# Optimization experiments

Measured on AMD Instinct MI355X. Metric: run time of the kernel, lower is better.

Reference implementation:

```python
import jax, jax.numpy as jnp
import numpy as np
from jax.experimental.ode import odeint

B, N, D, META, H, OUT = 512, 64, 4, 4, 512, 1
RTOL, ATOL = 1e-3, 1e-5


def setup_inputs() -> dict:
    key = jax.random.key(0)
    ks = jax.random.split(key, 20)
    # x channel 0 = strictly increasing event times per sample (TIME), rest randn
    dt = jax.random.uniform(ks[0], (B, N), dtype=jnp.float32) * 0.1 + 0.01
    times = jnp.cumsum(dt, axis=1)
    feats = jax.random.normal(ks[1], (B, N, D - 1), dtype=jnp.float32)
    x = jnp.concatenate([times[..., None], feats], axis=-1)
    meta = jax.random.normal(ks[2], (B, META), dtype=jnp.float32)
    eps = jax.random.normal(ks[3], (B, H), dtype=jnp.float32)

    DIN = D + META
    s_in = 1.0 / np.sqrt(DIN)
    s_h = 1.0 / np.sqrt(H)
    p = {
        # GRU (torch layout: gates [r, z, n] stacked)
        'gru_Wih': jax.random.normal(ks[4], (3 * H, DIN), jnp.float32) * s_in,
        'gru_Whh': jax.random.normal(ks[5], (3 * H, H), jnp.float32) * s_h,
        'gru_bih': jax.random.normal(ks[6], (3 * H,), jnp.float32) * s_h,
        'gru_bhh': jax.random.normal(ks[7], (3 * H,), jnp.float32) * s_h,
        # encoder head: Linear(H,H) -> ReLU -> Linear(H,2H)
        'enc_W1': jax.random.normal(ks[8], (H, H), jnp.float32) * s_h,
        'enc_b1': jax.random.normal(ks[9], (H,), jnp.float32) * s_h,
        'enc_W2': jax.random.normal(ks[10], (2 * H, H), jnp.float32) * s_h,
        'enc_b2': jax.random.normal(ks[11], (2 * H,), jnp.float32) * s_h,
        # ODE drift net: Linear(H,H) -> SELU -> Linear(H,H); scaled mild for stable dynamics
        'ode_W1': jax.random.normal(ks[12], (H, H), jnp.float32) * (0.5 * s_h),
        'ode_b1': jax.random.normal(ks[13], (H,), jnp.float32) * 0.05,
        'ode_W2': jax.random.normal(ks[14], (H, H), jnp.float32) * (0.5 * s_h),
        'ode_b2': jax.random.normal(ks[15], (H,), jnp.float32) * 0.05,
        # output head: Linear(H+META, OUT)
        'fc_W': jax.random.normal(ks[16], (OUT, H + META), jnp.float32) / np.sqrt(H + META),
        'fc_b': jax.random.normal(ks[17], (OUT,), jnp.float32) / np.sqrt(H + META),
    }
    return {'x': x, 'meta': meta, 'eps': eps, **p}


def _gru_last(xm, Wih, Whh, bih, bhh):
    # xm: (B, N, DIN) -> final hidden state (B, H), torch nn.GRU equations
    def step(h, x_t):
        gi = x_t @ Wih.T + bih            # (B, 3H)
        gh = h @ Whh.T + bhh              # (B, 3H)
        i_r, i_z, i_n = jnp.split(gi, 3, axis=-1)
        h_r, h_z, h_n = jnp.split(gh, 3, axis=-1)
        r = jax.nn.sigmoid(i_r + h_r)
        z = jax.nn.sigmoid(i_z + h_z)
        n = jnp.tanh(i_n + r * h_n)
        return (1.0 - z) * n + z * h, None
    h0 = jnp.zeros((xm.shape[0], Whh.shape[1]), xm.dtype)
    h, _ = jax.lax.scan(step, h0, jnp.swapaxes(xm, 0, 1))
    return h


def reference(x, meta, eps, gru_Wih, gru_Whh, gru_bih, gru_bhh,
              enc_W1, enc_b1, enc_W2, enc_b2,
              ode_W1, ode_b1, ode_W2, ode_b2, fc_W, fc_b):
    times = x[:, :, 0]                                        # (B, N)
    metat = jnp.broadcast_to(meta[:, None, :], (x.shape[0], x.shape[1], meta.shape[1]))
    xm = jnp.concatenate([x, metat], axis=-1)                 # (B, N, D+META)
    h = _gru_last(xm, gru_Wih, gru_Whh, gru_bih, gru_bhh)     # (B, H)
    out = jax.nn.relu(h @ enc_W1.T + enc_b1) @ enc_W2.T + enc_b2
    mean, std = out[:, :H], out[:, H:]
    z0 = eps * std + mean                                     # reparameterized sample

    def drift(z, t, W1, b1, W2, b2):
        return jax.nn.selu(z @ W1.T + b1) @ W2.T + b2

    def solve_one(z0_b, t_b):
        return odeint(drift, z0_b, t_b, ode_W1, ode_b1, ode_W2, ode_b2,
                      rtol=RTOL, atol=ATOL)                   # (N, H)

    solves = jax.vmap(solve_one)(z0, times)                   # (B, N, H)
    latent = jnp.concatenate([solves[:, -1, :], meta], axis=-1)
    return latent @ fc_W.T + fc_b                             # (B, OUT)
```

## Files before the change

### kernel.cpp

```cpp
#include <hip/hip_runtime.h>
#include <math.h>

constexpr int Bsz  = 512;
constexpr int Nseq = 64;
constexpr int DX   = 4;
constexpr int MET  = 4;
constexpr int Hd   = 512;
constexpr int H3d  = 1536;

constexpr int PJ = 520;

constexpr float RTOL_C = 1e-3f;
constexpr float ATOL_C = 1e-5f;

constexpr float SB10 = (float)(1.0/5.0);
constexpr float SB20 = (float)(3.0/40.0),  SB21 = (float)(9.0/40.0);
constexpr float SB30 = (float)(44.0/45.0), SB31 = (float)(-56.0/15.0), SB32 = (float)(32.0/9.0);
constexpr float SB40 = (float)(19372.0/6561.0), SB41 = (float)(-25360.0/2187.0),
                SB42 = (float)(64448.0/6561.0), SB43 = (float)(-212.0/729.0);
constexpr float SB50 = (float)(9017.0/3168.0),  SB51 = (float)(-355.0/33.0),
                SB52 = (float)(46732.0/5247.0), SB53 = (float)(49.0/176.0),
                SB54 = (float)(-5103.0/18656.0);
constexpr float CS0 = (float)(35.0/384.0), CS2 = (float)(500.0/1113.0),
                CS3 = (float)(125.0/192.0), CS4 = (float)(-2187.0/6784.0),
                CS5 = (float)(11.0/84.0);
constexpr float CE0 = (float)(35.0/384.0 - 1951.0/21600.0);
constexpr float CE2 = (float)(500.0/1113.0 - 22642.0/50085.0);
constexpr float CE3 = (float)(125.0/192.0 - 451.0/720.0);
constexpr float CE4 = (float)(-2187.0/6784.0 + 12231.0/42400.0);
constexpr float CE5 = (float)(11.0/84.0 - 649.0/6300.0);
constexpr float CE6 = (float)(-1.0/60.0);
constexpr float CM0 = (float)(6025192743.0/30085553152.0/2.0);
constexpr float CM2 = (float)(51252292925.0/65400821598.0/2.0);
constexpr float CM3 = (float)(-2691868925.0/45128329728.0/2.0);
constexpr float CM4 = (float)(187940372067.0/1594534317056.0/2.0);
constexpr float CM5 = (float)(-1776094331.0/19743644256.0/2.0);
constexpr float CM6 = (float)(11237099.0/235043384.0/2.0);

__device__ __forceinline__ float selu_f(float v) {
  const float scl = 1.0507009873554805f;
  const float alp = 1.6732632423543772f;
  float e = v > 0.f ? v : alp * expm1f(v);
  return scl * e;
}
__device__ __forceinline__ float sigmoid_f(float v) {
  return 1.f / (1.f + expf(-v));
}

__global__ __launch_bounds__(256) void pack_all_kernel(
    const float* __restrict__ gWhh, const float* __restrict__ gWih,
    const float* __restrict__ eW1,  const float* __restrict__ eW2,
    const float* __restrict__ oW1,  const float* __restrict__ oW2,
    float* __restrict__ WhhP, float* __restrict__ WihT,
    float* __restrict__ eW1P, float* __restrict__ eW2P,
    float* __restrict__ oW1P, float* __restrict__ oW2P)
{
  int i = blockIdx.x * 256 + threadIdx.x;
  if (i < 786432) {
    const int r = i >> 9, k = i & 511;
    const int gate = r >> 9, jr = r & 511;
    WhhP[(((k >> 2) * 3 + gate) * PJ + jr) * 4 + (k & 3)] = gWhh[i];
  } else if (i < 798720) {
    const int ii = i - 786432;
    const int r = ii >> 3, c = ii & 7;
    WihT[c * H3d + r] = gWih[ii];
  } else if (i < 1060864) {
    const int ii = i - 798720;
    const int r = ii >> 9, k = ii & 511;
    eW1P[(k >> 2) * (Hd * 4) + r * 4 + (k & 3)] = eW1[ii];
  } else if (i < 1585152) {
    const int ii = i - 1060864;
    const int r = ii >> 9, k = ii & 511;
    eW2P[(k >> 2) * (1024 * 4) + r * 4 + (k & 3)] = eW2[ii];
  } else if (i < 1847296) {
    const int ii = i - 1585152;
    const int r = ii >> 9, k = ii & 511;
    oW1P[((k >> 2) * PJ + r) * 4 + (k & 3)] = oW1[ii];
  } else if (i < 2109440) {
    const int ii = i - 1847296;
    const int r = ii >> 9, k = ii & 511;
    oW2P[((k >> 2) * PJ + r) * 4 + (k & 3)] = oW2[ii];
  }
}

__global__ __launch_bounds__(512) void gru_step_kernel(
    const float* __restrict__ x, const float* __restrict__ meta,
    const float* __restrict__ WihT, const float* __restrict__ WhhP,
    const float* __restrict__ bih, const float* __restrict__ bhh,
    const float* __restrict__ h_in, float* __restrict__ h_out, int t)
{
  __shared__ __align__(16) float hs[16 * Hd];
  const int tid = threadIdx.x;
  const int jl  = tid & 63;
  const int rg  = tid >> 6;
  const int j   = blockIdx.y * 64 + jl;
  const int b0  = blockIdx.x * 16;

  for (int i = tid; i < 16 * Hd / 4; i += 512)
    *(float4*)&hs[i * 4] = *(const float4*)&h_in[b0 * Hd + i * 4];
  __syncthreads();

  float ar0 = 0.f, az0 = 0.f, an0 = 0.f;
  float ar1 = 0.f, az1 = 0.f, an1 = 0.f;
#pragma unroll 4
  for (int k4 = 0; k4 < Hd / 4; ++k4) {
    const float4 wr = *(const float4*)&WhhP[((k4 * 3 + 0) * PJ + j) * 4];
    const float4 wz = *(const float4*)&WhhP[((k4 * 3 + 1) * PJ + j) * 4];
    const float4 wn = *(const float4*)&WhhP[((k4 * 3 + 2) * PJ + j) * 4];
    const float4 h0 = *(const float4*)&hs[(rg * 2 + 0) * Hd + k4 * 4];
    const float4 h1 = *(const float4*)&hs[(rg * 2 + 1) * Hd + k4 * 4];
    ar0 += wr.x * h0.x + wr.y * h0.y + wr.z * h0.z + wr.w * h0.w;
    az0 += wz.x * h0.x + wz.y * h0.y + wz.z * h0.z + wz.w * h0.w;
    an0 += wn.x * h0.x + wn.y * h0.y + wn.z * h0.z + wn.w * h0.w;
    ar1 += wr.x * h1.x + wr.y * h1.y + wr.z * h1.z + wr.w * h1.w;
    az1 += wz.x * h1.x + wz.y * h1.y + wz.z * h1.z + wz.w * h1.w;
    an1 += wn.x * h1.x + wn.y * h1.y + wn.z * h1.z + wn.w * h1.w;
  }

  const float bihr = bih[j], bihz = bih[512 + j], bihn = bih[1024 + j];
  const float bhhr = bhh[j], bhhz = bhh[512 + j], bhhn = bhh[1024 + j];
  float wir[8], wiz[8], win[8];
#pragma unroll
  for (int kk = 0; kk < 8; ++kk) {
    wir[kk] = WihT[kk * H3d + j];
    wiz[kk] = WihT[kk * H3d + 512 + j];
    win[kk] = WihT[kk * H3d + 1024 + j];
  }

#pragma unroll
  for (int m = 0; m < 2; ++m) {
    const int bl = rg * 2 + m;
    const int b  = b0 + bl;
    const float4 xv = *(const float4*)&x[(b * Nseq + t) * DX];
    const float4 mv = *(const float4*)&meta[b * MET];
    float xm[8] = { xv.x, xv.y, xv.z, xv.w, mv.x, mv.y, mv.z, mv.w };
    float gr = bihr, gz = bihz, gn = bihn;
#pragma unroll
    for (int kk = 0; kk < 8; ++kk) {
      gr += xm[kk] * wir[kk];
      gz += xm[kk] * wiz[kk];
      gn += xm[kk] * win[kk];
    }
    const float ghr = (m ? ar1 : ar0) + bhhr;
    const float ghz = (m ? az1 : az0) + bhhz;
    const float ghn = (m ? an1 : an0) + bhhn;
    const float r = sigmoid_f(gr + ghr);
    const float z = sigmoid_f(gz + ghz);
    const float n = tanhf(gn + r * ghn);
    const float hold = hs[bl * Hd + j];
    h_out[b * Hd + j] = (1.f - z) * n + z * hold;
  }
}

__global__ __launch_bounds__(256) void gemm_relu_kernel(
    const float* __restrict__ A, const float* __restrict__ WP,
    const float* __restrict__ bias, float* __restrict__ Cout)
{
  __shared__ __align__(16) float as[16 * Hd];
  const int tid  = threadIdx.x;
  const int jl   = tid & 63;
  const int bsub = tid >> 6;
  const int j    = blockIdx.y * 64 + jl;
  const int b0   = blockIdx.x * 16;

  for (int i = tid; i < 16 * Hd; i += 256) as[i] = A[b0 * Hd + i];
  __syncthreads();

  float acc[4] = {0.f, 0.f, 0.f, 0.f};
#pragma unroll 2
  for (int k4 = 0; k4 < Hd / 4; ++k4) {
    const float4 w = *(const float4*)&WP[(k4 * Hd + j) * 4];
#pragma unroll
    for (int m = 0; m < 4; ++m) {
      const float4 av = *(const float4*)&as[(bsub * 4 + m) * Hd + k4 * 4];
      acc[m] += w.x * av.x + w.y * av.y + w.z * av.z + w.w * av.w;
    }
  }
  const float bj = bias[j];
#pragma unroll
  for (int m = 0; m < 4; ++m) {
    const int b = b0 + bsub * 4 + m;
    float v = acc[m] + bj;
    Cout[b * Hd + j] = v > 0.f ? v : 0.f;
  }
}

__global__ __launch_bounds__(256) void enc2_z0_kernel(
    const float* __restrict__ O1, const float* __restrict__ W2P,
    const float* __restrict__ b2, const float* __restrict__ eps,
    float* __restrict__ z0)
{
  __shared__ __align__(16) float as[16 * Hd];
  const int tid  = threadIdx.x;
  const int jl   = tid & 63;
  const int bsub = tid >> 6;
  const int j    = blockIdx.y * 64 + jl;
  const int b0   = blockIdx.x * 16;

  for (int i = tid; i < 16 * Hd; i += 256) as[i] = O1[b0 * Hd + i];
  __syncthreads();

  float am[4] = {0.f, 0.f, 0.f, 0.f};
  float asd[4] = {0.f, 0.f, 0.f, 0.f};
#pragma unroll 2
  for (int k4 = 0; k4 < Hd / 4; ++k4) {
    const float4 wm = *(const float4*)&W2P[(k4 * 1024 + j) * 4];
    const float4 ws = *(const float4*)&W2P[(k4 * 1024 + 512 + j) * 4];
#pragma unroll
    for (int m = 0; m < 4; ++m) {
      const float4 av = *(const float4*)&as[(bsub * 4 + m) * Hd + k4 * 4];
      am[m]  += wm.x * av.x + wm.y * av.y + wm.z * av.z + wm.w * av.w;
      asd[m] += ws.x * av.x + ws.y * av.y + ws.z * av.z + ws.w * av.w;
    }
  }
  const float bm = b2[j], bs = b2[512 + j];
#pragma unroll
  for (int m = 0; m < 4; ++m) {
    const int b = b0 + bsub * 4 + m;
    const float mean = am[m] + bm;
    const float sd   = asd[m] + bs;
    z0[b * Hd + j] = eps[b * Hd + j] * sd + mean;
  }
}

__global__ __launch_bounds__(512) void ode_fc_kernel(
    const float* __restrict__ x, const float* __restrict__ meta,
    const float* __restrict__ z0in,
    const float* __restrict__ W1P, const float* __restrict__ b1v,
    const float* __restrict__ W2P, const float* __restrict__ b2v,
    const float* __restrict__ fcW, const float* __restrict__ fcb,
    float* __restrict__ outp)
{
  constexpr int GE = 2;
  __shared__ __align__(16) float zsh[GE][Hd];
  __shared__ float red[8 * GE];
  const int tid = threadIdx.x;
  const int jj  = tid & 255;
  const int eh  = tid >> 8;
  const int j1  = jj + 256;
  const int bg0 = blockIdx.x * GE;

  const float b1a = b1v[jj], b1b = b1v[j1];
  const float b2a = b2v[jj], b2b = b2v[j1];

  auto drift = [&](const float (&in)[2], float (&out)[2]) {
    __syncthreads();
    zsh[eh][jj] = in[0];
    zsh[eh][j1] = in[1];
    __syncthreads();
    float u0 = b1a, u1 = b1b;
#pragma unroll 4
    for (int k4 = 0; k4 < Hd / 4; ++k4) {
      const float4 wA = *(const float4*)&W1P[(k4 * PJ + jj) * 4];
      const float4 wB = *(const float4*)&W1P[(k4 * PJ + j1) * 4];
      const float4 z  = *(const float4*)&zsh[eh][k4 * 4];
      u0 += wA.x * z.x + wA.y * z.y + wA.z * z.z + wA.w * z.w;
      u1 += wB.x * z.x + wB.y * z.y + wB.z * z.z + wB.w * z.w;
    }
    u0 = selu_f(u0); u1 = selu_f(u1);
    __syncthreads();
    zsh[eh][jj] = u0;
    zsh[eh][j1] = u1;
    __syncthreads();
    float v0 = b2a, v1 = b2b;
#pragma unroll 4
    for (int k4 = 0; k4 < Hd / 4; ++k4) {
      const float4 wA = *(const float4*)&W2P[(k4 * PJ + jj) * 4];
      const float4 wB = *(const float4*)&W2P[(k4 * PJ + j1) * 4];
      const float4 z  = *(const float4*)&zsh[eh][k4 * 4];
      v0 += wA.x * z.x + wA.y * z.y + wA.z * z.z + wA.w * z.w;
      v1 += wB.x * z.x + wB.y * z.y + wB.z * z.z + wB.w * z.w;
    }
    out[0] = v0; out[1] = v1;
  };

  auto blocksum = [&](float (&v)[GE], float (&s)[GE]) {
#pragma unroll
    for (int off = 32; off > 0; off >>= 1) {
#pragma unroll
      for (int g = 0; g < GE; ++g) v[g] += __shfl_down(v[g], off);
    }
    __syncthreads();
    if ((tid & 63) == 0) {
      const int w = tid >> 6;
#pragma unroll
      for (int g = 0; g < GE; ++g) red[w * GE + g] = v[g];
    }
    __syncthreads();
#pragma unroll
    for (int g = 0; g < GE; ++g) {
      float t = 0.f;
#pragma unroll
      for (int w = 0; w < 8; ++w) t += red[w * GE + g];
      s[g] = t;
    }
  };

  float y[2], f[2], py[2], pf[2], ym[2];
  float tcur[GE], dtv[GE], tfin[GE], ptv[GE], pdt[GE];
  bool act[GE];

  y[0] = z0in[(bg0 + eh) * Hd + jj];
  y[1] = z0in[(bg0 + eh) * Hd + j1];
#pragma unroll
  for (int g = 0; g < GE; ++g) {
    tcur[g] = x[((bg0 + g) * Nseq + 0) * DX];
    tfin[g] = x[((bg0 + g) * Nseq + (Nseq - 1)) * DX];
  }

  drift(y, f);

  float sc[2];
  float q0[GE] = {0.f, 0.f}, q1[GE] = {0.f, 0.f};
#pragma unroll
  for (int l = 0; l < 2; ++l) {
    sc[l] = ATOL_C + RTOL_C * fabsf(y[l]);
    const float a = y[l] / sc[l], b = f[l] / sc[l];
    q0[eh] += a * a;
    q1[eh] += b * b;
  }
  float d0s[GE], d1s[GE];
  blocksum(q0, d0s);
  blocksum(q1, d1s);
  float h0[GE];
#pragma unroll
  for (int g = 0; g < GE; ++g) {
    const float d0 = sqrtf(d0s[g]), d1 = sqrtf(d1s[g]);
    h0[g] = (d0 < 1e-5f || d1 < 1e-5f) ? 1e-6f : 0.01f * d0 / d1;
  }
  float yin[2], f1h[2];
#pragma unroll
  for (int l = 0; l < 2; ++l) yin[l] = y[l] + h0[eh] * f[l];
  drift(yin, f1h);
  float q2[GE] = {0.f, 0.f};
#pragma unroll
  for (int l = 0; l < 2; ++l) {
    const float dd = (f1h[l] - f[l]) / sc[l];
    q2[eh] += dd * dd;
  }
  float d2s[GE];
  blocksum(q2, d2s);
#pragma unroll
  for (int g = 0; g < GE; ++g) {
    const float d1 = sqrtf(d1s[g]);
    const float d2 = sqrtf(d2s[g]) / h0[g];
    const float h1 = (d1 <= 1e-15f && d2 <= 1e-15f)
                 ? fmaxf(1e-6f, h0[g] * 1e-3f)
                 : powf(0.01f / (d1 + d2), 0.2f);
    dtv[g] = fminf(100.f * h0[g], h1);
    ptv[g] = tcur[g]; pdt[g] = dtv[g];
    act[g] = (tcur[g] < tfin[g]) && (dtv[g] > 0.f);
  }
#pragma unroll
  for (int l = 0; l < 2; ++l) { py[l] = y[l]; pf[l] = f[l]; ym[l] = y[l]; }

  float k2[2], k3[2], k4v[2], k5[2], k6[2], k7[2], y1v[2];
  for (int iter = 0; iter < 4000; ++iter) {
    if (!(act[0] || act[1])) break;

#pragma unroll
    for (int l = 0; l < 2; ++l) yin[l] = y[l] + dtv[eh] * (SB10 * f[l]);
    drift(yin, k2);

#pragma unroll
    for (int l = 0; l < 2; ++l)
      yin[l] = y[l] + dtv[eh] * (SB20 * f[l] + SB21 * k2[l]);
    drift(yin, k3);

#pragma unroll
    for (int l = 0; l < 2; ++l)
      yin[l] = y[l] + dtv[eh] * (SB30 * f[l] + SB31 * k2[l] + SB32 * k3[l]);
    drift(yin, k4v);

#pragma unroll
    for (int l = 0; l < 2; ++l)
      yin[l] = y[l] + dtv[eh] * (SB40 * f[l] + SB41 * k2[l] + SB42 * k3[l] + SB43 * k4v[l]);
    drift(yin, k5);

#pragma unroll
    for (int l = 0; l < 2; ++l)
      yin[l] = y[l] + dtv[eh] * (SB50 * f[l] + SB51 * k2[l] + SB52 * k3[l] + SB53 * k4v[l] + SB54 * k5[l]);
    drift(yin, k6);

#pragma unroll
    for (int l = 0; l < 2; ++l)
      y1v[l] = y[l] + dtv[eh] * (CS0 * f[l] + CS2 * k3[l] + CS3 * k4v[l] + CS4 * k5[l] + CS5 * k6[l]);
    drift(y1v, k7);

    float rs[GE] = {0.f, 0.f};
#pragma unroll
    for (int l = 0; l < 2; ++l) {
      const float yerr = dtv[eh] * (CE0 * f[l] + CE2 * k3[l] + CE3 * k4v[l] + CE4 * k5[l] + CE5 * k6[l] + CE6 * k7[l]);
      const float tol = ATOL_C + RTOL_C * fmaxf(fabsf(y[l]), fabsf(y1v[l]));
      const float r = yerr / tol;
      rs[eh] += r * r;
    }
    float rsum[GE];
    blocksum(rs, rsum);

    bool acc[GE];
#pragma unroll
    for (int g = 0; g < GE; ++g)
      acc[g] = act[g] && (sqrtf(rsum[g] * (1.0f / Hd)) <= 1.0f);

    if (acc[eh]) {
#pragma unroll
      for (int l = 0; l < 2; ++l) {
        ym[l] = y[l] + dtv[eh] * (CM0 * f[l] + CM2 * k3[l] + CM3 * k4v[l] + CM4 * k5[l] + CM5 * k6[l] + CM6 * k7[l]);
        py[l] = y[l]; pf[l] = f[l];
        y[l] = y1v[l]; f[l] = k7[l];
      }
    }
#pragma unroll
    for (int g = 0; g < GE; ++g) {
      if (!act[g]) continue;
      const float er = sqrtf(rsum[g] * (1.0f / Hd));
      if (acc[g]) {
        ptv[g] = tcur[g]; pdt[g] = dtv[g];
        tcur[g] = tcur[g] + dtv[g];
      }
      float dtn;
      if (er == 0.0f) {
        dtn = dtv[g] * 10.0f;
      } else {
        const float dfac = (er < 1.0f) ? 1.0f : 0.2f;
        const float fac = fminf(10.0f, fmaxf(0.9f * powf(er, -0.2f), dfac));
        dtn = dtv[g] * fac;
      }
      dtv[g] = fmaxf(dtn, 0.0f);
      act[g] = (tcur[g] < tfin[g]) && (dtv[g] > 0.0f);
    }
  }

  const float fcwA = fcW[jj];
  const float fcwB = fcW[j1];
  float s[GE] = {0.f, 0.f};
#pragma unroll
  for (int l = 0; l < 2; ++l) {
    const float denom = tcur[eh] - ptv[eh];
    const float xr = (tfin[eh] - ptv[eh]) / denom;
    const float dy0 = pdt[eh] * pf[l];
    const float dy1 = pdt[eh] * f[l];
    const float aa = -2.f * dy0 + 2.f * dy1 - 8.f * py[l] - 8.f * y[l] + 16.f * ym[l];
    const float bb =  5.f * dy0 - 3.f * dy1 + 18.f * py[l] + 14.f * y[l] - 32.f * ym[l];
    const float cc = -4.f * dy0 + 1.f * dy1 - 11.f * py[l] - 5.f * y[l] + 16.f * ym[l];
    const float dd = dy0;
    const float ee = py[l];
    const float yf = (((aa * xr + bb) * xr + cc) * xr + dd) * xr + ee;
    s[eh] += yf * ((l == 1) ? fcwB : fcwA);
  }
  float ssum[GE];
  blocksum(s, ssum);
  if (tid == 0) {
#pragma unroll
    for (int g = 0; g < GE; ++g) {
      float o = ssum[g] + fcb[0];
#pragma unroll
      for (int m = 0; m < MET; ++m) o += meta[(bg0 + g) * MET + m] * fcW[Hd + m];
      outp[bg0 + g] = o;
    }
  }
}

extern "C" void kernel_launch(void* const* d_in, const int* in_sizes, int n_in,
                              void* d_out, int out_size, void* d_ws, size_t ws_size,
                              hipStream_t stream)
{
  (void)in_sizes; (void)n_in; (void)out_size; (void)ws_size;

  const float* x    = (const float*)d_in[0];
  const float* meta = (const float*)d_in[1];
  const float* eps  = (const float*)d_in[2];
  const float* gWih = (const float*)d_in[3];
  const float* gWhh = (const float*)d_in[4];
  const float* gbih = (const float*)d_in[5];
  const float* gbhh = (const float*)d_in[6];
  const float* eW1  = (const float*)d_in[7];
  const float* eb1  = (const float*)d_in[8];
  const float* eW2  = (const float*)d_in[9];
  const float* eb2  = (const float*)d_in[10];
  const float* oW1  = (const float*)d_in[11];
  const float* ob1  = (const float*)d_in[12];
  const float* oW2  = (const float*)d_in[13];
  const float* ob2  = (const float*)d_in[14];
  const float* fcW  = (const float*)d_in[15];
  const float* fcb  = (const float*)d_in[16];
  float* out = (float*)d_out;
  float* ws  = (float*)d_ws;

  float* WhhP = ws + 0;
  float* WihT = ws + 798720;
  float* eW1P = ws + 811008;
  float* eW2P = ws + 1073152;
  float* oW1P = ws + 1597440;
  float* oW2P = ws + 1863680;
  float* hA   = ws + 2129920;
  float* hB   = ws + 2392064;

  pack_all_kernel<<<(2109440 + 255) / 256, 256, 0, stream>>>(
      gWhh, gWih, eW1, eW2, oW1, oW2, WhhP, WihT, eW1P, eW2P, oW1P, oW2P);
  hipMemsetAsync(hA, 0, (size_t)Bsz * Hd * sizeof(float), stream);

  dim3 ggrid(32, 8);
  for (int t = 0; t < Nseq; ++t) {
    const float* hin = (t & 1) ? hB : hA;
    float* hout      = (t & 1) ? hA : hB;
    gru_step_kernel<<<ggrid, 512, 0, stream>>>(x, meta, WihT, WhhP, gbih, gbhh, hin, hout, t);
  }
  dim3 egrid(32, 8);
  gemm_relu_kernel<<<egrid, 256, 0, stream>>>(hA, eW1P, eb1, hB);
  enc2_z0_kernel<<<egrid, 256, 0, stream>>>(hB, eW2P, eb2, eps, hA);
  ode_fc_kernel<<<Bsz / 2, 512, 0, stream>>>(x, meta, hA, oW1P, ob1, oW2P, ob2, fcW, fcb, out);
}
```

Baseline: 2.863 ms.

## Stage GRU weights in LDS and remap ODE threads to share weight loads

The GRU step kernel now double-buffers chunks of the r and z gate weights through shared memory and keeps the n gate read directly from global memory. The ODE kernel remaps threads so each thread owns one output column for both batch elements of the block. Each weight float4 is then loaded once and applied to two latent vectors instead of being loaded separately per sample. This halves global weight traffic in the drift matrix-vector products, which dominate runtime. The cost is more shared-memory reads of z and extra syncs in the GRU loop.

```diff
diff --git a/kernel.cpp b/kernel.cpp
--- a/kernel.cpp
+++ b/kernel.cpp
@@ -9,6 +9,7 @@
 constexpr int H3d  = 1536;
 
 constexpr int PJ = 520;
+constexpr int CK = 8;
 
 constexpr float RTOL_C = 1e-3f;
 constexpr float ATOL_C = 1e-5f;
@@ -90,31 +91,54 @@
     const float* __restrict__ h_in, float* __restrict__ h_out, int t)
 {
   __shared__ __align__(16) float hs[16 * Hd];
+  __shared__ __align__(16) float4 wlds[2][CK * 2 * 64];
   const int tid = threadIdx.x;
   const int jl  = tid & 63;
   const int rg  = tid >> 6;
-  const int j   = blockIdx.y * 64 + jl;
+  const int j0  = blockIdx.y * 64;
+  const int j   = j0 + jl;
   const int b0  = blockIdx.x * 16;
+
+  const float4* __restrict__ W4 = (const float4*)WhhP;
 
   for (int i = tid; i < 16 * Hd / 4; i += 512)
     *(float4*)&hs[i * 4] = *(const float4*)&h_in[b0 * Hd + i * 4];
+
+  auto stage = [&](int c, int buf) {
+    for (int i = tid; i < CK * 2 * 64; i += 512) {
+      const int kk   = i >> 7;
+      const int rem  = i & 127;
+      const int gate = rem >> 6;
+      const int col  = rem & 63;
+      wlds[buf][i] = W4[((c * CK + kk) * 3 + gate) * PJ + j0 + col];
+    }
+  };
+  stage(0, 0);
   __syncthreads();
 
   float ar0 = 0.f, az0 = 0.f, an0 = 0.f;
   float ar1 = 0.f, az1 = 0.f, an1 = 0.f;
-#pragma unroll 4
-  for (int k4 = 0; k4 < Hd / 4; ++k4) {
-    const float4 wr = *(const float4*)&WhhP[((k4 * 3 + 0) * PJ + j) * 4];
-    const float4 wz = *(const float4*)&WhhP[((k4 * 3 + 1) * PJ + j) * 4];
-    const float4 wn = *(const float4*)&WhhP[((k4 * 3 + 2) * PJ + j) * 4];
-    const float4 h0 = *(const float4*)&hs[(rg * 2 + 0) * Hd + k4 * 4];
-    const float4 h1 = *(const float4*)&hs[(rg * 2 + 1) * Hd + k4 * 4];
-    ar0 += wr.x * h0.x + wr.y * h0.y + wr.z * h0.z + wr.w * h0.w;
-    az0 += wz.x * h0.x + wz.y * h0.y + wz.z * h0.z + wz.w * h0.w;
-    an0 += wn.x * h0.x + wn.y * h0.y + wn.z * h0.z + wn.w * h0.w;
-    ar1 += wr.x * h1.x + wr.y * h1.y + wr.z * h1.z + wr.w * h1.w;
-    az1 += wz.x * h1.x + wz.y * h1.y + wz.z * h1.z + wz.w * h1.w;
-    an1 += wn.x * h1.x + wn.y * h1.y + wn.z * h1.z + wn.w * h1.w;
+  constexpr int NCHUNK = (Hd / 4) / CK;
+  for (int c = 0; c < NCHUNK; ++c) {
+    const int buf = c & 1;
+    if (c + 1 < NCHUNK) stage(c + 1, buf ^ 1);
+    const float4* __restrict__ wl = &wlds[buf][0];
+#pragma unroll
+    for (int kk = 0; kk < CK; ++kk) {
+      const int k4 = c * CK + kk;
+      const float4 wr = wl[(kk * 2 + 0) * 64 + jl];
+      const float4 wz = wl[(kk * 2 + 1) * 64 + jl];
+      const float4 wn = W4[(k4 * 3 + 2) * PJ + j];
+      const float4 h0 = *(const float4*)&hs[(rg * 2 + 0) * Hd + k4 * 4];
+      const float4 h1 = *(const float4*)&hs[(rg * 2 + 1) * Hd + k4 * 4];
+      ar0 += wr.x * h0.x + wr.y * h0.y + wr.z * h0.z + wr.w * h0.w;
+      az0 += wz.x * h0.x + wz.y * h0.y + wz.z * h0.z + wz.w * h0.w;
+      an0 += wn.x * h0.x + wn.y * h0.y + wn.z * h0.z + wn.w * h0.w;
+      ar1 += wr.x * h1.x + wr.y * h1.y + wr.z * h1.z + wr.w * h1.w;
+      az1 += wz.x * h1.x + wz.y * h1.y + wz.z * h1.z + wz.w * h1.w;
+      an1 += wn.x * h1.x + wn.y * h1.y + wn.z * h1.z + wn.w * h1.w;
+    }
+    __syncthreads();
   }
 
   const float bihr = bih[j], bihz = bih[512 + j], bihn = bih[1024 + j];
@@ -235,41 +259,39 @@
   __shared__ __align__(16) float zsh[GE][Hd];
   __shared__ float red[8 * GE];
   const int tid = threadIdx.x;
-  const int jj  = tid & 255;
-  const int eh  = tid >> 8;
-  const int j1  = jj + 256;
+  const int j   = tid;
   const int bg0 = blockIdx.x * GE;
 
-  const float b1a = b1v[jj], b1b = b1v[j1];
-  const float b2a = b2v[jj], b2b = b2v[j1];
+  const float b1r = b1v[j];
+  const float b2r = b2v[j];
 
   auto drift = [&](const float (&in)[2], float (&out)[2]) {
     __syncthreads();
-    zsh[eh][jj] = in[0];
-    zsh[eh][j1] = in[1];
-    __syncthreads();
-    float u0 = b1a, u1 = b1b;
+    zsh[0][j] = in[0];
+    zsh[1][j] = in[1];
+    __syncthreads();
+    float u0 = b1r, u1 = b1r;
 #pragma unroll 4
     for (int k4 = 0; k4 < Hd / 4; ++k4) {
-      const float4 wA = *(const float4*)&W1P[(k4 * PJ + jj) * 4];
-      const float4 wB = *(const float4*)&W1P[(k4 * PJ + j1) * 4];
-      const float4 z  = *(const float4*)&zsh[eh][k4 * 4];
-      u0 += wA.x * z.x + wA.y * z.y + wA.z * z.z + wA.w * z.w;
-      u1 += wB.x * z.x + wB.y * z.y + wB.z * z.z + wB.w * z.w;
+      const float4 w  = *(const float4*)&W1P[(k4 * PJ + j) * 4];
+      const float4 z0 = *(const float4*)&zsh[0][k4 * 4];
+      const float4 z1 = *(const float4*)&zsh[1][k4 * 4];
+      u0 += w.x * z0.x + w.y * z0.y + w.z * z0.z + w.w * z0.w;
+      u1 += w.x * z1.x + w.y * z1.y + w.z * z1.z + w.w * z1.w;
     }
     u0 = selu_f(u0); u1 = selu_f(u1);
     __syncthreads();
-    zsh[eh][jj] = u0;
-    zsh[eh][j1] = u1;
-    __syncthreads();
-    float v0 = b2a, v1 = b2b;
+    zsh[0][j] = u0;
+    zsh[1][j] = u1;
+    __syncthreads();
+    float v0 = b2r, v1 = b2r;
 #pragma unroll 4
     for (int k4 = 0; k4 < Hd / 4; ++k4) {
-      const float4 wA = *(const float4*)&W2P[(k4 * PJ + jj) * 4];
-      const float4 wB = *(const float4*)&W2P[(k4 * PJ + j1) * 4];
-      const float4 z  = *(const float4*)&zsh[eh][k4 * 4];
-      v0 += wA.x * z.x + wA.y * z.y + wA.z * z.z + wA.w * z.w;
-      v1 += wB.x * z.x + wB.y * z.y + wB.z * z.z + wB.w * z.w;
+      const float4 w  = *(const float4*)&W2P[(k4 * PJ + j) * 4];
+      const float4 z0 = *(const float4*)&zsh[0][k4 * 4];
+      const float4 z1 = *(const float4*)&zsh[1][k4 * 4];
+      v0 += w.x * z0.x + w.y * z0.y + w.z * z0.z + w.w * z0.w;
+      v1 += w.x * z1.x + w.y * z1.y + w.z * z1.z + w.w * z1.w;
     }
     out[0] = v0; out[1] = v1;
   };
@@ -300,24 +322,22 @@
   float tcur[GE], dtv[GE], tfin[GE], ptv[GE], pdt[GE];
   bool act[GE];
 
-  y[0] = z0in[(bg0 + eh) * Hd + jj];
-  y[1] = z0in[(bg0 + eh) * Hd + j1];
 #pragma unroll
   for (int g = 0; g < GE; ++g) {
+    y[g]    = z0in[(bg0 + g) * Hd + j];
     tcur[g] = x[((bg0 + g) * Nseq + 0) * DX];
     tfin[g] = x[((bg0 + g) * Nseq + (Nseq - 1)) * DX];
   }
 
   drift(y, f);
 
-  float sc[2];
-  float q0[GE] = {0.f, 0.f}, q1[GE] = {0.f, 0.f};
+  float sc[2], q0[GE], q1[GE];
 #pragma unroll
   for (int l = 0; l < 2; ++l) {
     sc[l] = ATOL_C + RTOL_C * fabsf(y[l]);
     const float a = y[l] / sc[l], b = f[l] / sc[l];
-    q0[eh] += a * a;
-    q1[eh] += b * b;
+    q0[l] = a * a;
+    q1[l] = b * b;
   }
   float d0s[GE], d1s[GE];
   blocksum(q0, d0s);
@@ -330,13 +350,13 @@
   }
   float yin[2], f1h[2];
 #pragma unroll
-  for (int l = 0; l < 2; ++l) yin[l] = y[l] + h0[eh] * f[l];
+  for (int l = 0; l < 2; ++l) yin[l] = y[l] + h0[l] * f[l];
   drift(yin, f1h);
-  float q2[GE] = {0.f, 0.f};
+  float q2[GE];
 #pragma unroll
   for (int l = 0; l < 2; ++l) {
     const float dd = (f1h[l] - f[l]) / sc[l];
-    q2[eh] += dd * dd;
+    q2[l] = dd * dd;
   }
   float d2s[GE];
   blocksum(q2, d2s);
@@ -359,41 +379,41 @@
     if (!(act[0] || act[1])) break;
 
 #pragma unroll
-    for (int l = 0; l < 2; ++l) yin[l] = y[l] + dtv[eh] * (SB10 * f[l]);
+    for (int l = 0; l < 2; ++l) yin[l] = y[l] + dtv[l] * (SB10 * f[l]);
     drift(yin, k2);
 
 #pragma unroll
     for (int l = 0; l < 2; ++l)
-      yin[l] = y[l] + dtv[eh] * (SB20 * f[l] + SB21 * k2[l]);
+      yin[l] = y[l] + dtv[l] * (SB20 * f[l] + SB21 * k2[l]);
     drift(yin, k3);
 
 #pragma unroll
     for (int l = 0; l < 2; ++l)
-      yin[l] = y[l] + dtv[eh] * (SB30 * f[l] + SB31 * k2[l] + SB32 * k3[l]);
+      yin[l] = y[l] + dtv[l] * (SB30 * f[l] + SB31 * k2[l] + SB32 * k3[l]);
     drift(yin, k4v);
 
 #pragma unroll
     for (int l = 0; l < 2; ++l)
-      yin[l] = y[l] + dtv[eh] * (SB40 * f[l] + SB41 * k2[l] + SB42 * k3[l] + SB43 * k4v[l]);
+      yin[l] = y[l] + dtv[l] * (SB40 * f[l] + SB41 * k2[l] + SB42 * k3[l] + SB43 * k4v[l]);
     drift(yin, k5);
 
 #pragma unroll
     for (int l = 0; l < 2; ++l)
-      yin[l] = y[l] + dtv[eh] * (SB50 * f[l] + SB51 * k2[l] + SB52 * k3[l] + SB53 * k4v[l] + SB54 * k5[l]);
+      yin[l] = y[l] + dtv[l] * (SB50 * f[l] + SB51 * k2[l] + SB52 * k3[l] + SB53 * k4v[l] + SB54 * k5[l]);
     drift(yin, k6);
 
 #pragma unroll
     for (int l = 0; l < 2; ++l)
-      y1v[l] = y[l] + dtv[eh] * (CS0 * f[l] + CS2 * k3[l] + CS3 * k4v[l] + CS4 * k5[l] + CS5 * k6[l]);
+      y1v[l] = y[l] + dtv[l] * (CS0 * f[l] + CS2 * k3[l] + CS3 * k4v[l] + CS4 * k5[l] + CS5 * k6[l]);
     drift(y1v, k7);
 
-    float rs[GE] = {0.f, 0.f};
+    float rs[GE];
 #pragma unroll
     for (int l = 0; l < 2; ++l) {
-      const float yerr = dtv[eh] * (CE0 * f[l] + CE2 * k3[l] + CE3 * k4v[l] + CE4 * k5[l] + CE5 * k6[l] + CE6 * k7[l]);
+      const float yerr = dtv[l] * (CE0 * f[l] + CE2 * k3[l] + CE3 * k4v[l] + CE4 * k5[l] + CE5 * k6[l] + CE6 * k7[l]);
       const float tol = ATOL_C + RTOL_C * fmaxf(fabsf(y[l]), fabsf(y1v[l]));
       const float r = yerr / tol;
-      rs[eh] += r * r;
+      rs[l] = r * r;
     }
     float rsum[GE];
     blocksum(rs, rsum);
@@ -403,10 +423,10 @@
     for (int g = 0; g < GE; ++g)
       acc[g] = act[g] && (sqrtf(rsum[g] * (1.0f / Hd)) <= 1.0f);
 
-    if (acc[eh]) {
-#pragma unroll
-      for (int l = 0; l < 2; ++l) {
-        ym[l] = y[l] + dtv[eh] * (CM0 * f[l] + CM2 * k3[l] + CM3 * k4v[l] + CM4 * k5[l] + CM5 * k6[l] + CM6 * k7[l]);
+#pragma unroll
+    for (int l = 0; l < 2; ++l) {
+      if (acc[l]) {
+        ym[l] = y[l] + dtv[l] * (CM0 * f[l] + CM2 * k3[l] + CM3 * k4v[l] + CM4 * k5[l] + CM5 * k6[l] + CM6 * k7[l]);
         py[l] = y[l]; pf[l] = f[l];
         y[l] = y1v[l]; f[l] = k7[l];
       }
@@ -432,22 +452,21 @@
     }
   }
 
-  const float fcwA = fcW[jj];
-  const float fcwB = fcW[j1];
-  float s[GE] = {0.f, 0.f};
+  const float fcw = fcW[j];
+  float s[GE];
 #pragma unroll
   for (int l = 0; l < 2; ++l) {
-    const float denom = tcur[eh] - ptv[eh];
-    const float xr = (tfin[eh] - ptv[eh]) / denom;
-    const float dy0 = pdt[eh] * pf[l];
-    const float dy1 = pdt[eh] * f[l];
+    const float denom = tcur[l] - ptv[l];
+    const float xr = (tfin[l] - ptv[l]) / denom;
+    const float dy0 = pdt[l] * pf[l];
+    const float dy1 = pdt[l] * f[l];
     const float aa = -2.f * dy0 + 2.f * dy1 - 8.f * py[l] - 8.f * y[l] + 16.f * ym[l];
     const float bb =  5.f * dy0 - 3.f * dy1 + 18.f * py[l] + 14.f * y[l] - 32.f * ym[l];
     const float cc = -4.f * dy0 + 1.f * dy1 - 11.f * py[l] - 5.f * y[l] + 16.f * ym[l];
     const float dd = dy0;
     const float ee = py[l];
     const float yf = (((aa * xr + bb) * xr + cc) * xr + dd) * xr + ee;
-    s[eh] += yf * ((l == 1) ? fcwB : fcwA);
+    s[l] = yf * fcw;
   }
   float ssum[GE];
   blocksum(s, ssum);
```

Measured after the change: 2.752 ms. -3.9%, faster.
